# Kernel tuning notes

Hardware: AMD Instinct MI355X
Metric: run time of the kernel (lower is better)

The kernel has to match this reference:

```python
import jax, jax.numpy as jnp
import numpy as np

N = 4096
F_IN = 128
N_HEADS = 4
N_HIDDEN = 16  # out_features 64 // 4 heads
LRELU_SLOPE = 0.2


def setup_inputs() -> dict:
    key = jax.random.key(0)
    k1, k2, k3 = jax.random.split(key, 3)
    x = jax.random.normal(k1, (N, F_IN), dtype=jnp.float32)
    adj = jax.random.randint(jax.random.fold_in(key, 7), (N, N), 0, 2, dtype=jnp.int32)
    # linearinput weight: in_features -> n_heads * n_hidden (no bias)
    W = jax.random.normal(k2, (F_IN, N_HEADS * N_HIDDEN), dtype=jnp.float32) / np.sqrt(F_IN)
    # attn weight: 2*n_hidden -> 1 (no bias), shared across heads
    attn_w = jax.random.normal(k3, (2 * N_HIDDEN,), dtype=jnp.float32) / np.sqrt(2 * N_HIDDEN)
    return {"x": x, "adj": adj, "W": W, "attn_w": attn_w}


def reference(x, adj, W, attn_w):
    n = x.shape[0]
    # h: (N, H, Dh)
    h = (x @ W).reshape(n, N_HEADS, N_HIDDEN)
    # attn is linear on [h_i || h_j] => e_ij = lrelu(src_i + dst_j)
    a_src = attn_w[:N_HIDDEN]
    a_dst = attn_w[N_HIDDEN:]
    src = jnp.einsum('nhd,d->nh', h, a_src)  # (N, H)
    dst = jnp.einsum('nhd,d->nh', h, a_dst)  # (N, H)
    e = jax.nn.leaky_relu(src[:, None, :] + dst[None, :, :], negative_slope=LRELU_SLOPE)  # (N, N, H)
    a = jax.nn.softmax(e, axis=1)  # softmax over neighbor axis j
    # dropout in eval mode: identity
    attn_res = jnp.einsum('ijh,jhf->ihf', a, h)  # (N, H, Dh)
    return attn_res.reshape(n, N_HEADS * N_HIDDEN)  # is_concat=True
```

## Files before the change

kernel.cpp:

```cpp
#include <hip/hip_runtime.h>

#define NN 4096
#define FIN 128
#define NHEAD 4
#define NHID 16
#define NCOL 64
#define SLOPE 0.2f
#define CHUNK 64
#define NCH 64
#define NCOLS 17
#define RPAD 20

__device__ __forceinline__ float lrelu(float v){ return v > 0.f ? v : SLOPE * v; }

__device__ __forceinline__ unsigned fkey(float f){
  unsigned b = __float_as_uint(f);
  return b ^ ((b & 0x80000000u) ? 0xFFFFFFFFu : 0x80000000u);
}
__device__ __forceinline__ float fkey_inv(unsigned k){
  unsigned b = (k & 0x80000000u) ? (k ^ 0x80000000u) : ~k;
  return __uint_as_float(b);
}

__global__ __launch_bounds__(256) void gemm_h_k(const float* __restrict__ x,
                                                const float* __restrict__ W,
                                                const float* __restrict__ aw,
                                                float* __restrict__ h,
                                                float* __restrict__ src,
                                                float* __restrict__ dst){
  __shared__ __align__(16) float wl[FIN][NCOL];
  __shared__ float xlT[FIN][10];
  __shared__ float hs[8][NCOL + 1];
  int t = threadIdx.x;
  int row0 = blockIdx.x * 8;
  for (int k4 = t; k4 < FIN * NCOL / 4; k4 += 256)
    ((float4*)&wl[0][0])[k4] = ((const float4*)W)[k4];
  for (int k = t; k < 8 * FIN; k += 256){
    int r = k >> 7, d = k & 127;
    xlT[d][r] = x[(row0 + r) * FIN + d];
  }
  __syncthreads();
  int col = t & 63, rb = t >> 6;
  float a0 = 0.f, a1 = 0.f;
  #pragma unroll
  for (int d = 0; d < FIN; ++d){
    float wv = wl[d][col];
    float2 xv = *(const float2*)&xlT[d][rb * 2];
    a0 = fmaf(xv.x, wv, a0);
    a1 = fmaf(xv.y, wv, a1);
  }
  h[(row0 + rb * 2) * NCOL + col] = a0;     hs[rb * 2][col] = a0;
  h[(row0 + rb * 2 + 1) * NCOL + col] = a1; hs[rb * 2 + 1][col] = a1;
  __syncthreads();
  if (t < 32){
    int r = t >> 2, hd = t & 3;
    float s = 0.f, d = 0.f;
    #pragma unroll
    for (int f = 0; f < NHID; ++f){
      float v = hs[r][hd * NHID + f];
      s = fmaf(v, aw[f], s);
      d = fmaf(v, aw[NHID + f], d);
    }
    src[hd * NN + row0 + r] = s;
    dst[hd * NN + row0 + r] = d;
  }
}

__global__ __launch_bounds__(256) void ranksc_k(const float* __restrict__ dst,
                                                unsigned long long* __restrict__ ksort,
                                                unsigned* __restrict__ dkey){
  int ib = blockIdx.x;
  int hd = blockIdx.y;
  __shared__ __align__(16) unsigned long long keys[8 * 514];
  int t = threadIdx.x;
  const float* dp = dst + hd * NN;
  for (int j = t; j < NN; j += 256)
    keys[(j >> 9) * 514 + (j & 511)] =
        ((unsigned long long)fkey(dp[j]) << 32) | (unsigned)j;
  __syncthreads();
  int il = t >> 3, jseg = t & 7;
  int i = ib * 32 + il;
  unsigned long long my = keys[(i >> 9) * 514 + (i & 511)];
  const ulonglong2* kp2 = (const ulonglong2*)&keys[jseg * 514];
  int cnt = 0;
  #pragma unroll 8
  for (int q = 0; q < 256; ++q){
    ulonglong2 kk = kp2[q];
    cnt += (kk.x < my) ? 1 : 0;
    cnt += (kk.y < my) ? 1 : 0;
  }
  cnt += __shfl_down(cnt, 4);
  cnt += __shfl_down(cnt, 2);
  cnt += __shfl_down(cnt, 1);
  if (jseg == 0){
    ksort[hd * NN + cnt] = my;
    dkey[hd * NN + cnt]  = (unsigned)(my >> 32);
  }
}

__global__ __launch_bounds__(256) void scanA_k(const float* __restrict__ h,
                                               const unsigned long long* __restrict__ ksort,
                                               float* __restrict__ PL2,
                                               float* __restrict__ SL2,
                                               float* __restrict__ ctP,
                                               float* __restrict__ ctS){
  int ch = blockIdx.x;
  int hd = blockIdx.y;
  int t = threadIdx.x;
  int base = ch * CHUNK;
  __shared__ float e02[CHUNK], e1[CHUNK];
  __shared__ int   pms[CHUNK];
  __shared__ float hl[CHUNK][RPAD];
  __shared__ float PLs[CHUNK][RPAD], SLs[CHUNK][RPAD];
  if (t < CHUNK){
    unsigned long long key = ksort[hd * NN + base + t];
    float d = fkey_inv((unsigned)(key >> 32));
    e02[t] = __expf(0.2f * d);
    e1[t]  = __expf(d);
    pms[t] = (int)(unsigned)key;
    hl[t][16] = 1.0f;
  }
  __syncthreads();
  {
    int col = t & 15, r0 = t >> 4;
    #pragma unroll
    for (int it = 0; it < 4; ++it){
      int r = it * 16 + r0;
      hl[r][col] = h[pms[r] * NCOL + hd * NHID + col];
    }
  }
  __syncthreads();
  if (t < NCOLS){
    int col = t;
    float run = 0.f;
    #pragma unroll
    for (int r = 0; r < CHUNK; ++r){
      PLs[r][col] = run;
      run = fmaf(e02[r], hl[r][col], run);
    }
    ctP[ch * 68 + hd * 17 + col] = run;
  } else if (t >= 64 && t < 64 + NCOLS){
    int col = t - 64;
    float rs = 0.f;
    #pragma unroll
    for (int r = CHUNK - 1; r >= 0; --r){
      rs = fmaf(e1[r], hl[r][col], rs);
      SLs[r][col] = rs;
    }
    ctS[ch * 68 + hd * 17 + col] = rs;
  }
  __syncthreads();
  #pragma unroll
  for (int n = 0; n < 5; ++n){
    int idx = n * 256 + t;
    int r = idx / RPAD, c = idx % RPAD;
    PL2[(hd * NN + base + r) * RPAD + c] = PLs[r][c];
    SL2[(hd * NN + base + r) * RPAD + c] = SLs[r][c];
  }
}

__global__ __launch_bounds__(256) void out_k(const float* __restrict__ src,
                                             const unsigned* __restrict__ dkey,
                                             const float* __restrict__ PL2,
                                             const float* __restrict__ SL2,
                                             const float* __restrict__ ctP,
                                             const float* __restrict__ ctS,
                                             float* __restrict__ out){
  __shared__ __align__(16) unsigned dk[NN];
  __shared__ __align__(16) float oP[NCH + 1][68];
  __shared__ __align__(16) float oS[NCH][68];
  int t = threadIdx.x;
  int hd = blockIdx.x & 3, ig = blockIdx.x >> 2;
  const unsigned* dkp = dkey + hd * NN;
  #pragma unroll
  for (int n = 0; n < 4; ++n)
    ((uint4*)dk)[n * 256 + t] = ((const uint4*)dkp)[n * 256 + t];
  #pragma unroll
  for (int n = 0; n < 5; ++n){
    int idx = n * 256 + t;
    if (idx < 1088){
      ((float4*)&oP[0][0])[idx] = ((const float4*)ctP)[idx];
      ((float4*)&oS[0][0])[idx] = ((const float4*)ctS)[idx];
    }
  }
  __syncthreads();
  if (t < 68){
    float run = 0.f;
    #pragma unroll
    for (int c = 0; c < NCH; ++c){ float v = oP[c][t]; oP[c][t] = run; run += v; }
    oP[NCH][t] = run;
  } else if (t >= 128 && t < 196){
    int cc = t - 128;
    float rs = 0.f;
    #pragma unroll
    for (int c = NCH - 1; c >= 0; --c){ float v = oS[c][cc]; oS[c][cc] = rs; rs += v; }
  }
  __syncthreads();
  int p = t >> 2, q = t & 3;
  int i = ig * 64 + p;
  float s = src[hd * NN + i];
  unsigned tu = fkey(-s);
  int lo = 0, hi = NN;
  while (lo < hi){
    int mid = (lo + hi) >> 1;
    if (dk[mid] < tu) lo = mid + 1; else hi = mid;
  }
  int k = lo;
  float4 res;
  if (k == NN){
    float inv = 1.0f / oP[NCH][hd * 17 + 16];
    res.x = oP[NCH][hd * 17 + q * 4 + 0] * inv;
    res.y = oP[NCH][hd * 17 + q * 4 + 1] * inv;
    res.z = oP[NCH][hd * 17 + q * 4 + 2] * inv;
    res.w = oP[NCH][hd * 17 + q * 4 + 3] * inv;
  } else {
    float dmax = fkey_inv(dk[NN - 1]);
    float m = lrelu(s + dmax);
    float alpha = __expf(0.2f * s - m);
    float beta  = __expf(s - m);
    int ch = k >> 6;
    const float* P2 = PL2 + (size_t)(hd * NN + k) * RPAD;
    const float* S2 = SL2 + (size_t)(hd * NN + k) * RPAD;
    float4 p4 = *(const float4*)(P2 + q * 4);
    float4 s4 = *(const float4*)(S2 + q * 4);
    float den = alpha * (P2[16] + oP[ch][hd * 17 + 16])
              + beta  * (S2[16] + oS[ch][hd * 17 + 16]);
    float inv = 1.0f / den;
    res.x = (alpha * (p4.x + oP[ch][hd * 17 + q * 4 + 0])
           + beta  * (s4.x + oS[ch][hd * 17 + q * 4 + 0])) * inv;
    res.y = (alpha * (p4.y + oP[ch][hd * 17 + q * 4 + 1])
           + beta  * (s4.y + oS[ch][hd * 17 + q * 4 + 1])) * inv;
    res.z = (alpha * (p4.z + oP[ch][hd * 17 + q * 4 + 2])
           + beta  * (s4.z + oS[ch][hd * 17 + q * 4 + 2])) * inv;
    res.w = (alpha * (p4.w + oP[ch][hd * 17 + q * 4 + 3])
           + beta  * (s4.w + oS[ch][hd * 17 + q * 4 + 3])) * inv;
  }
  *(float4*)(out + i * NCOL + hd * NHID + q * 4) = res;
}

extern "C" void kernel_launch(void* const* d_in, const int* in_sizes, int n_in,
                              void* d_out, int out_size, void* d_ws, size_t ws_size,
                              hipStream_t stream){
  const float* x  = (const float*)d_in[0];
  const float* W  = (const float*)d_in[2];
  const float* aw = (const float*)d_in[3];
  float* out = (float*)d_out;
  float* ws  = (float*)d_ws;

  float*              h     = ws;
  float*              src   = ws + 262144;
  float*              dst   = ws + 278528;
  unsigned long long* ksort = (unsigned long long*)(ws + 294912);
  unsigned*           dkey  = (unsigned*)(ws + 327680);
  float*              PL2   = ws + 344064;
  float*              SL2   = ws + 671744;
  float*              ctP   = ws + 999424;
  float*              ctS   = ws + 1003776;

  gemm_h_k<<<512, 256, 0, stream>>>(x, W, aw, h, src, dst);
  ranksc_k<<<dim3(128, NHEAD), 256, 0, stream>>>(dst, ksort, dkey);
  scanA_k<<<dim3(NCH, NHEAD), 256, 0, stream>>>(h, ksort, PL2, SL2, ctP, ctS);
  out_k<<<256, 256, 0, stream>>>(src, dkey, PL2, SL2, ctP, ctS, out);
}
```

Before: 33.54 us.

## Register-block rank counting so each thread ranks eight keys per LDS load

Rewrites the rank-sort kernel so each thread holds eight target keys in registers and compares them against a 64-key segment, with each loaded LDS key reused eight times. Blocks grow to 512 threads and handle 64 ranks each, halving the grid. Partial counts are reduced across lanes with shuffles and across waves through a small shared table. This aims to cut LDS bandwidth per comparison, at the cost of more registers and an extra block barrier.

Result: faster. 28.55 us (-14.9%).

```diff
diff --git a/kernel.cpp b/kernel.cpp
--- a/kernel.cpp
+++ b/kernel.cpp
@@ -66,35 +66,52 @@
   }
 }
 
-__global__ __launch_bounds__(256) void ranksc_k(const float* __restrict__ dst,
+__global__ __launch_bounds__(512) void ranksc_k(const float* __restrict__ dst,
                                                 unsigned long long* __restrict__ ksort,
                                                 unsigned* __restrict__ dkey){
   int ib = blockIdx.x;
   int hd = blockIdx.y;
-  __shared__ __align__(16) unsigned long long keys[8 * 514];
+  __shared__ __align__(16) unsigned long long keys2[64][66];
+  __shared__ int wsum[8][64];
   int t = threadIdx.x;
   const float* dp = dst + hd * NN;
-  for (int j = t; j < NN; j += 256)
-    keys[(j >> 9) * 514 + (j & 511)] =
-        ((unsigned long long)fkey(dp[j]) << 32) | (unsigned)j;
-  __syncthreads();
-  int il = t >> 3, jseg = t & 7;
-  int i = ib * 32 + il;
-  unsigned long long my = keys[(i >> 9) * 514 + (i & 511)];
-  const ulonglong2* kp2 = (const ulonglong2*)&keys[jseg * 514];
-  int cnt = 0;
-  #pragma unroll 8
-  for (int q = 0; q < 256; ++q){
-    ulonglong2 kk = kp2[q];
-    cnt += (kk.x < my) ? 1 : 0;
-    cnt += (kk.y < my) ? 1 : 0;
-  }
-  cnt += __shfl_down(cnt, 4);
-  cnt += __shfl_down(cnt, 2);
-  cnt += __shfl_down(cnt, 1);
-  if (jseg == 0){
-    ksort[hd * NN + cnt] = my;
-    dkey[hd * NN + cnt]  = (unsigned)(my >> 32);
+  for (int j = t; j < NN; j += 512)
+    keys2[j >> 6][j & 63] = ((unsigned long long)fkey(dp[j]) << 32) | (unsigned)j;
+  __syncthreads();
+  int g = t >> 3, c = t & 7;
+  unsigned long long mk[8];
+  #pragma unroll
+  for (int r = 0; r < 8; ++r) mk[r] = keys2[ib][c * 8 + r];
+  int cnt[8] = {0, 0, 0, 0, 0, 0, 0, 0};
+  const ulonglong2* kp = (const ulonglong2*)&keys2[g][0];
+  #pragma unroll 4
+  for (int q = 0; q < 32; ++q){
+    ulonglong2 kk = kp[q];
+    #pragma unroll
+    for (int r = 0; r < 8; ++r){
+      cnt[r] += (kk.x < mk[r]) ? 1 : 0;
+      cnt[r] += (kk.y < mk[r]) ? 1 : 0;
+    }
+  }
+  #pragma unroll
+  for (int r = 0; r < 8; ++r){
+    cnt[r] += __shfl_down(cnt[r], 32);
+    cnt[r] += __shfl_down(cnt[r], 16);
+    cnt[r] += __shfl_down(cnt[r], 8);
+  }
+  int w = t >> 6;
+  if ((t & 63) < 8){
+    #pragma unroll
+    for (int r = 0; r < 8; ++r) wsum[w][c * 8 + r] = cnt[r];
+  }
+  __syncthreads();
+  if (t < 64){
+    int rank = 0;
+    #pragma unroll
+    for (int w2 = 0; w2 < 8; ++w2) rank += wsum[w2][t];
+    unsigned long long key = keys2[ib][t];
+    ksort[hd * NN + rank] = key;
+    dkey[hd * NN + rank]  = (unsigned)(key >> 32);
   }
 }
 
@@ -258,7 +275,7 @@
   float*              ctS   = ws + 1003776;
 
   gemm_h_k<<<512, 256, 0, stream>>>(x, W, aw, h, src, dst);
-  ranksc_k<<<dim3(128, NHEAD), 256, 0, stream>>>(dst, ksort, dkey);
+  ranksc_k<<<dim3(64, NHEAD), 512, 0, stream>>>(dst, ksort, dkey);
   scanA_k<<<dim3(NCH, NHEAD), 256, 0, stream>>>(h, ksort, PL2, SL2, ctP, ctS);
   out_k<<<256, 256, 0, stream>>>(src, dkey, PL2, SL2, ctP, ctS, out);
 }
```
